# Kernel optimization log

Measured on AMD Instinct MI355X. Metric: run time of the kernel, lower is better.

Reference implementation:

```python
import jax, jax.numpy as jnp
import numpy as np

DILATIONS = [1, 2, 4, 8, 16, 32, 64, 128]
HIDDEN = 128
BATCH = 256
N_STEPS = 784
N_CLASSES = 10


def _drnn_layer(x_tbd, W_ih, W_hh, b_ih, b_hh, rate):
    """Dilated RNN layer. x_tbd: (T, B, D). Returns (T, B, H).

    Faithful to the repo's dRNN: pad T to a multiple of rate with zeros,
    fold each group of `rate` consecutive timesteps into the batch dim,
    step a tanh RNNCell over T/rate dilated steps (zero init state),
    then un-interleave back to (T, B, H).
    """
    T, B, D = x_tbd.shape
    n_dil = -(-T // rate)  # ceil division
    pad = n_dil * rate - T
    xp = jnp.pad(x_tbd, ((0, pad), (0, 0), (0, 0)))
    # (n_dil, rate*B, D): torch.cat of rate consecutive steps along batch
    xd = xp.reshape(n_dil, rate * B, D)

    def step(h, xt):
        h_new = jnp.tanh(xt @ W_ih.T + b_ih + h @ W_hh.T + b_hh)
        return h_new, h_new

    h0 = jnp.zeros((rate * B, W_ih.shape[0]), dtype=x_tbd.dtype)
    _, outs = jax.lax.scan(step, h0, xd)  # (n_dil, rate*B, H)
    outs = outs.reshape(n_dil * rate, B, -1)[:T]  # un-interleave, drop pad
    return outs


def _forward(x, Wih0, Whh0, bih0, bhh0, Wih, Whh, bih, bhh, W, b):
    # x: (B, T, D) -> time-major (T, B, D), matching _rnn_reformat
    h = jnp.transpose(x, (1, 0, 2))
    h = _drnn_layer(h, Wih0, Whh0, bih0, bhh0, DILATIONS[0])
    for i, rate in enumerate(DILATIONS[1:]):
        h = _drnn_layer(h, Wih[i], Whh[i], bih[i], bhh[i], rate)
    # dilations[0] == 1 branch: logits from last timestep of last layer
    return h[-1] @ W + b  # (B, n_classes)


def setup_inputs() -> dict:
    key = jax.random.key(0)
    ks = jax.random.split(key, 12)
    s = 0.05  # keep tanh in its linear-ish range
    return {
        "x": jax.random.normal(ks[0], (BATCH, N_STEPS, 1), jnp.float32),
        "Wih0": jax.random.normal(ks[1], (HIDDEN, 1), jnp.float32) * s,
        "Whh0": jax.random.normal(ks[2], (HIDDEN, HIDDEN), jnp.float32) * s,
        "bih0": jax.random.normal(ks[3], (HIDDEN,), jnp.float32) * s,
        "bhh0": jax.random.normal(ks[4], (HIDDEN,), jnp.float32) * s,
        "Wih": jax.random.normal(ks[5], (7, HIDDEN, HIDDEN), jnp.float32) * s,
        "Whh": jax.random.normal(ks[6], (7, HIDDEN, HIDDEN), jnp.float32) * s,
        "bih": jax.random.normal(ks[7], (7, HIDDEN), jnp.float32) * s,
        "bhh": jax.random.normal(ks[8], (7, HIDDEN), jnp.float32) * s,
        "W": jax.random.normal(ks[9], (HIDDEN, N_CLASSES), jnp.float32),
        "b": jax.random.normal(ks[10], (N_CLASSES,), jnp.float32),
    }


def reference(x, Wih0, Whh0, bih0, bhh0, Wih, Whh, bih, bhh, W, b):
    return _forward(x, Wih0, Whh0, bih0, bhh0, Wih, Whh, bih, bhh, W, b)
```

## Files before the change

kernel.cpp:

```cpp
#include <hip/hip_runtime.h>


typedef __attribute__((ext_vector_type(8))) short bf16x8;
typedef __attribute__((ext_vector_type(4))) float f32x4;
typedef __attribute__((ext_vector_type(2))) unsigned int u32x2;
typedef __attribute__((ext_vector_type(2))) unsigned long long u64x2;

#define TSTEPS 784
#define NBATCH 256
#define HID 128
#define SLOT_ELEMS (NBATCH * HID)
#define XPITCH 788
#define DYN_LDS 86016

struct Params {
  const float* x0;
  const float* Wih[8];
  const float* Whh[8];
  const float* bih[8];
  const float* bhh[8];
  unsigned short* phi[8];
  unsigned short* plo[8];
  float* hlast;
  int* flags;
  int jmax[8];
  int wpar[8];
  int sigb[8];
};

__device__ __forceinline__ unsigned short f32_to_bf16(float f) {
  unsigned int u = __builtin_bit_cast(unsigned int, f);
  u = (u + 0x7FFFu + ((u >> 16) & 1u)) >> 16;
  return (unsigned short)u;
}
__device__ __forceinline__ float bf16_to_f32(unsigned short s) {
  unsigned int u = ((unsigned int)s) << 16;
  return __builtin_bit_cast(float, u);
}
__device__ __forceinline__ void lds_barrier() {
  asm volatile("s_waitcnt lgkmcnt(0)" ::: "memory");
  __builtin_amdgcn_s_barrier();
  asm volatile("" ::: "memory");
}
__device__ __forceinline__ void load_wfrag(const float* __restrict__ p, bf16x8& hi, bf16x8& lo) {
#pragma unroll
  for (int i = 0; i < 8; ++i) {
    float v = p[i];
    unsigned short h = f32_to_bf16(v);
    float rem = v - bf16_to_f32(h);
    hi[i] = (short)h;
    lo[i] = (short)f32_to_bf16(rem);
  }
}

__global__ __launch_bounds__(256, 1) void drnn_fused(Params P) {
  extern __shared__ __align__(16) char smem[];
  unsigned short (*Hhi)[16][136] = (unsigned short(*)[16][136])smem;
  unsigned short (*Hlo)[16][136] = (unsigned short(*)[16][136])(smem + 8704);
  float* xlds = (float*)(smem + 17408);

  const int layer  = blockIdx.x >> 4;
  const int bg     = blockIdx.x & 15;
  const bool isL0   = (layer == 0);
  const bool isLast = (layer == 7);
  const int jmax = P.jmax[layer];
  const int wpar = P.wpar[layer];
  const int SIGB = P.sigb[layer];
  const float* __restrict__ Wih = P.Wih[layer];
  const float* __restrict__ Whh = P.Whh[layer];
  const float* __restrict__ bih = P.bih[layer];
  const float* __restrict__ bhh = P.bhh[layer];
  const unsigned short* __restrict__ Yin_hi = isL0 ? nullptr : P.phi[layer - 1];
  const unsigned short* __restrict__ Yin_lo = isL0 ? nullptr : P.plo[layer - 1];
  unsigned short* __restrict__ Yout_hi = isLast ? nullptr : P.phi[layer];
  unsigned short* __restrict__ Yout_lo = isLast ? nullptr : P.plo[layer];
  int* fin  = isL0 ? nullptr : P.flags + 64 * ((layer - 1) * 16 + bg);
  int* fout = isLast ? nullptr : P.flags + 64 * (layer * 16 + bg);

  const int tid  = threadIdx.x;
  const int wave = tid >> 6;
  const int lane = tid & 63;
  const int lrow = lane & 15;
  const int lgrp = lane >> 4;
  const int b0   = bg << 4;

  int seen = 0;
  auto wait_in = [&](int need) {
    if (seen >= need) return;
    while ((seen = __hip_atomic_load(fin, __ATOMIC_RELAXED,
                                     __HIP_MEMORY_SCOPE_SYSTEM)) < need)
      __builtin_amdgcn_s_sleep(2);
  };

  bf16x8 whhh[2][4], whhl[2][4], wihh[2][4], wihl[2][4];
#pragma unroll
  for (int tl = 0; tl < 2; ++tl) {
    const float* wp = Whh + (size_t)(wave * 32 + tl * 16 + lrow) * HID + lgrp * 8;
#pragma unroll
    for (int kb = 0; kb < 4; ++kb)
      load_wfrag(wp + kb * 32, whhh[tl][kb], whhl[tl][kb]);
  }
  if (!isL0) {
#pragma unroll
    for (int tl = 0; tl < 2; ++tl) {
      const float* wp = Wih + (size_t)(wave * 32 + tl * 16 + lrow) * HID + lgrp * 8;
#pragma unroll
      for (int kb = 0; kb < 4; ++kb)
        load_wfrag(wp + kb * 32, wihh[tl][kb], wihl[tl][kb]);
    }
  }
  f32x4 bias_[2], w0_[2];
#pragma unroll
  for (int tl = 0; tl < 2; ++tl)
#pragma unroll
    for (int r = 0; r < 4; ++r) {
      const int n = wave * 32 + tl * 16 + lgrp * 4 + r;
      bias_[tl][r] = bih[n] + bhh[n];
      w0_[tl][r]   = isL0 ? Wih[n] : 0.0f;
    }

  if (isL0) {
    for (int r = 0; r < 16; ++r)
      for (int i = tid; i < TSTEPS / 4; i += 256)
        *(f32x4*)&xlds[r * XPITCH + i * 4] =
            *(const f32x4*)&P.x0[(size_t)(b0 + r) * TSTEPS + i * 4];
    __syncthreads();
  }

  bf16x8 xhA[4], xlA[4], xhB[4], xlB[4];
  float xvA = 0.f, xvB = 0.f;
  const unsigned short* pin_h = nullptr;
  const unsigned short* pin_l = nullptr;
  if (isL0) {
    xvA = xlds[lrow * XPITCH + 0];
  } else {
    wait_in(1);
    const size_t lofs = ((size_t)b0 + lrow) * HID + lgrp * 8;
    pin_h = Yin_hi + lofs;
    pin_l = Yin_lo + lofs;
#pragma unroll
    for (int kb = 0; kb < 4; ++kb) {
      xhA[kb] = *(const bf16x8*)(pin_h + kb * 32);
      xlA[kb] = *(const bf16x8*)(pin_l + kb * 32);
    }
    pin_h += SLOT_ELEMS;
    pin_l += SLOT_ELEMS;
  }

  unsigned long long* wb_h = nullptr;
  unsigned long long* wb_l = nullptr;
  if (!isLast) {
    const int row = tid >> 4, cb = tid & 15;
    const size_t wofs = ((size_t)b0 + row) * HID + cb * 8;
    wb_h = (unsigned long long*)(Yout_hi + wofs);
    wb_l = (unsigned long long*)(Yout_lo + wofs);
  }
  const int wsrc = (tid >> 4) * 136 + (tid & 15) * 8;
  auto writeback = [&](int rp) {
    u64x2 vh = *(const u64x2*)((const unsigned short*)&Hhi[rp][0][0] + wsrc);
    u64x2 vl = *(const u64x2*)((const unsigned short*)&Hlo[rp][0][0] + wsrc);
    __hip_atomic_store(wb_h,     vh[0], __ATOMIC_RELAXED, __HIP_MEMORY_SCOPE_SYSTEM);
    __hip_atomic_store(wb_h + 1, vh[1], __ATOMIC_RELAXED, __HIP_MEMORY_SCOPE_SYSTEM);
    __hip_atomic_store(wb_l,     vl[0], __ATOMIC_RELAXED, __HIP_MEMORY_SCOPE_SYSTEM);
    __hip_atomic_store(wb_l + 1, vl[1], __ATOMIC_RELAXED, __HIP_MEMORY_SCOPE_SYSTEM);
    wb_h += SLOT_ELEMS / 4;
    wb_l += SLOT_ELEMS / 4;
  };
  auto signal = [&](int val) {
    asm volatile("s_waitcnt vmcnt(0)" ::: "memory");
    __builtin_amdgcn_s_barrier();
    if (tid == 0)
      __hip_atomic_store(fout, val, __ATOMIC_RELAXED, __HIP_MEMORY_SCOPE_SYSTEM);
  };

  int next_sig = SIGB;

  auto step = [&](int j, bf16x8 (&xh_c)[4], bf16x8 (&xl_c)[4],
                  bf16x8 (&xh_n)[4], bf16x8 (&xl_n)[4],
                  float& xv_c, float& xv_n) {
    if (j + 1 < jmax) {
      if (isL0) {
        xv_n = xlds[lrow * XPITCH + (j + 1)];
      } else {
        wait_in(j + 2);
#pragma unroll
        for (int kb = 0; kb < 4; ++kb) {
          xh_n[kb] = *(const bf16x8*)(pin_h + kb * 32);
          xl_n[kb] = *(const bf16x8*)(pin_l + kb * 32);
        }
        pin_h += SLOT_ELEMS;
        pin_l += SLOT_ELEMS;
      }
    }
    f32x4 c0[2], c1[2], c2[2];
#pragma unroll
    for (int tl = 0; tl < 2; ++tl) {
      c0[tl] = bias_[tl];
      c1[tl] = f32x4{0.f, 0.f, 0.f, 0.f};
      c2[tl] = f32x4{0.f, 0.f, 0.f, 0.f};
    }
    if (!isL0) {
#pragma unroll
      for (int kb = 0; kb < 4; ++kb)
#pragma unroll
        for (int tl = 0; tl < 2; ++tl) {
          c0[tl] = __builtin_amdgcn_mfma_f32_16x16x32_bf16(wihh[tl][kb], xh_c[kb], c0[tl], 0, 0, 0);
          c1[tl] = __builtin_amdgcn_mfma_f32_16x16x32_bf16(wihl[tl][kb], xh_c[kb], c1[tl], 0, 0, 0);
          c2[tl] = __builtin_amdgcn_mfma_f32_16x16x32_bf16(wihh[tl][kb], xl_c[kb], c2[tl], 0, 0, 0);
        }
    }
    if (j > 0) {
      lds_barrier();
      const int rp = (j - 1) & 1;
      bf16x8 bh[4], bl[4];
#pragma unroll
      for (int kb = 0; kb < 4; ++kb) {
        bh[kb] = *(const bf16x8*)&Hhi[rp][lrow][kb * 32 + lgrp * 8];
        bl[kb] = *(const bf16x8*)&Hlo[rp][lrow][kb * 32 + lgrp * 8];
      }
      if (!isLast && ((j - 1) & 1) == wpar) {
        const int wbslot = (j - 1 - wpar) >> 1;
        if (wbslot == next_sig) {
          signal(wbslot);
          next_sig += SIGB;
        }
        writeback(rp);
      }
#pragma unroll
      for (int kb = 0; kb < 4; ++kb)
#pragma unroll
        for (int tl = 0; tl < 2; ++tl) {
          c0[tl] = __builtin_amdgcn_mfma_f32_16x16x32_bf16(whhh[tl][kb], bh[kb], c0[tl], 0, 0, 0);
          c1[tl] = __builtin_amdgcn_mfma_f32_16x16x32_bf16(whhl[tl][kb], bh[kb], c1[tl], 0, 0, 0);
          c2[tl] = __builtin_amdgcn_mfma_f32_16x16x32_bf16(whhh[tl][kb], bl[kb], c2[tl], 0, 0, 0);
        }
    }
    const int pp = j & 1;
#pragma unroll
    for (int tl = 0; tl < 2; ++tl) {
      float y[4];
      f32x4 yv;
#pragma unroll
      for (int r = 0; r < 4; ++r) {
        float v = c0[tl][r] + c1[tl][r] + c2[tl][r];
        if (isL0) v = __builtin_fmaf(xv_c, w0_[tl][r], v);
        float t  = __builtin_amdgcn_exp2f(v * 2.885390081777927f);
        float rc = __builtin_amdgcn_rcpf(t + 1.0f);
        y[r] = __builtin_fmaf(-2.0f, rc, 1.0f);
        yv[r] = y[r];
      }
      float rem[4];
#pragma unroll
      for (int r = 0; r < 4; ++r) {
        float hf = __builtin_bit_cast(float,
            __builtin_bit_cast(unsigned int, y[r]) & 0xffff0000u);
        rem[r] = y[r] - hf;
      }
      u32x2 ph, pl;
      ph[0] = __builtin_amdgcn_perm(__builtin_bit_cast(unsigned int, y[1]),
                                    __builtin_bit_cast(unsigned int, y[0]), 0x07060302u);
      ph[1] = __builtin_amdgcn_perm(__builtin_bit_cast(unsigned int, y[3]),
                                    __builtin_bit_cast(unsigned int, y[2]), 0x07060302u);
      pl[0] = __builtin_amdgcn_perm(__builtin_bit_cast(unsigned int, rem[1]),
                                    __builtin_bit_cast(unsigned int, rem[0]), 0x07060302u);
      pl[1] = __builtin_amdgcn_perm(__builtin_bit_cast(unsigned int, rem[3]),
                                    __builtin_bit_cast(unsigned int, rem[2]), 0x07060302u);
      const int nb = wave * 32 + tl * 16 + lgrp * 4;
      *(u32x2*)&Hhi[pp][lrow][nb] = ph;
      *(u32x2*)&Hlo[pp][lrow][nb] = pl;
      if (isLast && j == jmax - 1)
        *(f32x4*)&P.hlast[(size_t)(b0 + lrow) * HID + nb] = yv;
    }
  };

  int j = 0;
  for (;;) {
    step(j, xhA, xlA, xhB, xlB, xvA, xvB);
    if (++j >= jmax) break;
    step(j, xhB, xlB, xhA, xlA, xvB, xvA);
    if (++j >= jmax) break;
  }

  if (!isLast) {
    if (((jmax - 1) & 1) == wpar) {
      lds_barrier();
      writeback((jmax - 1) & 1);
    }
    signal(((jmax - 1 - wpar) >> 1) + 1);
  }
}

__global__ __launch_bounds__(256) void logits_kernel(
    const float* __restrict__ hlast, const float* __restrict__ W,
    const float* __restrict__ bvec, float* __restrict__ out)
{
  __shared__ float Ws[HID * 10];
  const int tid = threadIdx.x;
  for (int i = tid; i < HID * 10; i += 256) Ws[i] = W[i];
  __syncthreads();
  float acc[10];
#pragma unroll
  for (int n = 0; n < 10; ++n) acc[n] = bvec[n];
  const float* h = hlast + (size_t)tid * HID;
#pragma unroll 4
  for (int k = 0; k < HID; ++k) {
    const float hv = h[k];
#pragma unroll
    for (int n = 0; n < 10; ++n) acc[n] += hv * Ws[k * 10 + n];
  }
#pragma unroll
  for (int n = 0; n < 10; ++n) out[(size_t)tid * 10 + n] = acc[n];
}

extern "C" void kernel_launch(void* const* d_in, const int* in_sizes, int n_in,
                              void* d_out, int out_size, void* d_ws, size_t ws_size,
                              hipStream_t stream) {
  (void)in_sizes; (void)n_in; (void)out_size; (void)ws_size;
  const float* x    = (const float*)d_in[0];
  const float* Wih0 = (const float*)d_in[1];
  const float* Whh0 = (const float*)d_in[2];
  const float* bih0 = (const float*)d_in[3];
  const float* bhh0 = (const float*)d_in[4];
  const float* WihA = (const float*)d_in[5];
  const float* WhhA = (const float*)d_in[6];
  const float* bihA = (const float*)d_in[7];
  const float* bhhA = (const float*)d_in[8];
  const float* Wout = (const float*)d_in[9];
  const float* bout = (const float*)d_in[10];
  float* out = (float*)d_out;

  static const int jmaxs[8] = {784, 392, 196, 98, 49, 25, 13, 7};
  static const int wpars[8] = {1, 1, 1, 1, 0, 0, 0, 0};
  static const int sigbs[8] = {8, 8, 8, 8, 4, 2, 2, 0};

  Params P;
  P.x0 = x;
  P.Wih[0] = Wih0; P.Whh[0] = Whh0; P.bih[0] = bih0; P.bhh[0] = bhh0;
  for (int i = 0; i < 7; ++i) {
    P.Wih[i + 1] = WihA + (size_t)i * HID * HID;
    P.Whh[i + 1] = WhhA + (size_t)i * HID * HID;
    P.bih[i + 1] = bihA + (size_t)i * HID;
    P.bhh[i + 1] = bhhA + (size_t)i * HID;
  }
  for (int i = 0; i < 8; ++i) {
    P.jmax[i] = jmaxs[i]; P.wpar[i] = wpars[i]; P.sigb[i] = sigbs[i];
  }

  unsigned short* wsp = (unsigned short*)d_ws;
  size_t off = 0;
  for (int i = 0; i < 7; ++i) {
    const size_t slots = (size_t)jmaxs[i + 1] * NBATCH * HID;
    P.phi[i] = wsp + off; off += slots;
    P.plo[i] = wsp + off; off += slots;
  }
  P.phi[7] = nullptr; P.plo[7] = nullptr;
  P.hlast = (float*)(wsp + off); off += (size_t)NBATCH * HID * 2;
  int* flags = (int*)(wsp + off);
  P.flags = flags;

  hipFuncSetAttribute((const void*)drnn_fused,
                      hipFuncAttributeMaxDynamicSharedMemorySize, DYN_LDS);

  hipMemsetAsync(flags, 0, 7 * 16 * 64 * sizeof(int), stream);
  drnn_fused<<<dim3(128), dim3(256), DYN_LDS, stream>>>(P);
  logits_kernel<<<dim3(1), dim3(256), 0, stream>>>(P.hlast, Wout, bout, out);
}
```

Baseline: 961.5 us.

## Switch recurrent MFMAs from split-bf16 3-pass to fp16 2-pass

Replaces the bf16 hi/lo split scheme (three MFMAs per tile: Whi*xhi, Wlo*xhi, Whi*xlo) with fp16 weights and an fp16 hi/lo split of activations only (two MFMAs per tile). Activations are split into fp16 hi plus fp16 residual, which works because tanh outputs and small weights fit fp16 range. The accumulators are regrouped per k-block into four independent chains to shorten MFMA dependency chains, and the hidden-state MFMAs are moved ahead of the writeback. This cuts MFMA count on the serial recurrence critical path and drops the low-part weight registers, at the cost of fp16 weight rounding precision.

```diff
diff --git a/kernel.cpp b/kernel.cpp
--- a/kernel.cpp
+++ b/kernel.cpp
@@ -1,9 +1,9 @@
 #include <hip/hip_runtime.h>
 
 
-typedef __attribute__((ext_vector_type(8))) short bf16x8;
+typedef __attribute__((ext_vector_type(8))) _Float16 f16x8;
+typedef __attribute__((ext_vector_type(4))) _Float16 f16x4;
 typedef __attribute__((ext_vector_type(4))) float f32x4;
-typedef __attribute__((ext_vector_type(2))) unsigned int u32x2;
 typedef __attribute__((ext_vector_type(2))) unsigned long long u64x2;
 
 #define TSTEPS 784
@@ -28,29 +28,21 @@
   int sigb[8];
 };
 
-__device__ __forceinline__ unsigned short f32_to_bf16(float f) {
-  unsigned int u = __builtin_bit_cast(unsigned int, f);
-  u = (u + 0x7FFFu + ((u >> 16) & 1u)) >> 16;
-  return (unsigned short)u;
-}
-__device__ __forceinline__ float bf16_to_f32(unsigned short s) {
-  unsigned int u = ((unsigned int)s) << 16;
-  return __builtin_bit_cast(float, u);
-}
 __device__ __forceinline__ void lds_barrier() {
   asm volatile("s_waitcnt lgkmcnt(0)" ::: "memory");
   __builtin_amdgcn_s_barrier();
   asm volatile("" ::: "memory");
 }
-__device__ __forceinline__ void load_wfrag(const float* __restrict__ p, bf16x8& hi, bf16x8& lo) {
-#pragma unroll
-  for (int i = 0; i < 8; ++i) {
-    float v = p[i];
-    unsigned short h = f32_to_bf16(v);
-    float rem = v - bf16_to_f32(h);
-    hi[i] = (short)h;
-    lo[i] = (short)f32_to_bf16(rem);
-  }
+__device__ __forceinline__ float tanh_fast(float v) {
+  float t  = __builtin_amdgcn_exp2f(v * 2.885390081777927f);
+  float rc = __builtin_amdgcn_rcpf(t + 1.0f);
+  return __builtin_fmaf(-2.0f, rc, 1.0f);
+}
+__device__ __forceinline__ f16x8 load_wf16(const float* __restrict__ p) {
+  f16x8 w;
+#pragma unroll
+  for (int i = 0; i < 8; ++i) w[i] = (_Float16)p[i];
+  return w;
 }
 
 __global__ __launch_bounds__(256, 1) void drnn_fused(Params P) {
@@ -92,13 +84,13 @@
       __builtin_amdgcn_s_sleep(2);
   };
 
-  bf16x8 whhh[2][4], whhl[2][4], wihh[2][4], wihl[2][4];
+  f16x8 whh[2][4], wih[2][4];
 #pragma unroll
   for (int tl = 0; tl < 2; ++tl) {
     const float* wp = Whh + (size_t)(wave * 32 + tl * 16 + lrow) * HID + lgrp * 8;
 #pragma unroll
     for (int kb = 0; kb < 4; ++kb)
-      load_wfrag(wp + kb * 32, whhh[tl][kb], whhl[tl][kb]);
+      whh[tl][kb] = load_wf16(wp + kb * 32);
   }
   if (!isL0) {
 #pragma unroll
@@ -106,7 +98,7 @@
       const float* wp = Wih + (size_t)(wave * 32 + tl * 16 + lrow) * HID + lgrp * 8;
 #pragma unroll
       for (int kb = 0; kb < 4; ++kb)
-        load_wfrag(wp + kb * 32, wihh[tl][kb], wihl[tl][kb]);
+        wih[tl][kb] = load_wf16(wp + kb * 32);
     }
   }
   f32x4 bias_[2], w0_[2];
@@ -127,7 +119,7 @@
     __syncthreads();
   }
 
-  bf16x8 xhA[4], xlA[4], xhB[4], xlB[4];
+  f16x8 xhA[4], xlA[4], xhB[4], xlB[4];
   float xvA = 0.f, xvB = 0.f;
   const unsigned short* pin_h = nullptr;
   const unsigned short* pin_l = nullptr;
@@ -140,8 +132,8 @@
     pin_l = Yin_lo + lofs;
 #pragma unroll
     for (int kb = 0; kb < 4; ++kb) {
-      xhA[kb] = *(const bf16x8*)(pin_h + kb * 32);
-      xlA[kb] = *(const bf16x8*)(pin_l + kb * 32);
+      xhA[kb] = *(const f16x8*)(pin_h + kb * 32);
+      xlA[kb] = *(const f16x8*)(pin_l + kb * 32);
     }
     pin_h += SLOT_ELEMS;
     pin_l += SLOT_ELEMS;
@@ -175,8 +167,8 @@
 
   int next_sig = SIGB;
 
-  auto step = [&](int j, bf16x8 (&xh_c)[4], bf16x8 (&xl_c)[4],
-                  bf16x8 (&xh_n)[4], bf16x8 (&xl_n)[4],
+  auto step = [&](int j, f16x8 (&xh_c)[4], f16x8 (&xl_c)[4],
+                  f16x8 (&xh_n)[4], f16x8 (&xl_n)[4],
                   float& xv_c, float& xv_n) {
     if (j + 1 < jmax) {
       if (isL0) {
@@ -185,39 +177,46 @@
         wait_in(j + 2);
 #pragma unroll
         for (int kb = 0; kb < 4; ++kb) {
-          xh_n[kb] = *(const bf16x8*)(pin_h + kb * 32);
-          xl_n[kb] = *(const bf16x8*)(pin_l + kb * 32);
+          xh_n[kb] = *(const f16x8*)(pin_h + kb * 32);
+          xl_n[kb] = *(const f16x8*)(pin_l + kb * 32);
         }
         pin_h += SLOT_ELEMS;
         pin_l += SLOT_ELEMS;
       }
     }
-    f32x4 c0[2], c1[2], c2[2];
+    f32x4 c[2][4];
 #pragma unroll
     for (int tl = 0; tl < 2; ++tl) {
-      c0[tl] = bias_[tl];
-      c1[tl] = f32x4{0.f, 0.f, 0.f, 0.f};
-      c2[tl] = f32x4{0.f, 0.f, 0.f, 0.f};
+      c[tl][0] = bias_[tl];
+#pragma unroll
+      for (int kb = 1; kb < 4; ++kb) c[tl][kb] = f32x4{0.f, 0.f, 0.f, 0.f};
     }
     if (!isL0) {
 #pragma unroll
       for (int kb = 0; kb < 4; ++kb)
 #pragma unroll
         for (int tl = 0; tl < 2; ++tl) {
-          c0[tl] = __builtin_amdgcn_mfma_f32_16x16x32_bf16(wihh[tl][kb], xh_c[kb], c0[tl], 0, 0, 0);
-          c1[tl] = __builtin_amdgcn_mfma_f32_16x16x32_bf16(wihl[tl][kb], xh_c[kb], c1[tl], 0, 0, 0);
-          c2[tl] = __builtin_amdgcn_mfma_f32_16x16x32_bf16(wihh[tl][kb], xl_c[kb], c2[tl], 0, 0, 0);
+          c[tl][kb] = __builtin_amdgcn_mfma_f32_16x16x32_f16(wih[tl][kb], xh_c[kb], c[tl][kb], 0, 0, 0);
+          c[tl][kb] = __builtin_amdgcn_mfma_f32_16x16x32_f16(wih[tl][kb], xl_c[kb], c[tl][kb], 0, 0, 0);
         }
     }
     if (j > 0) {
       lds_barrier();
       const int rp = (j - 1) & 1;
-      bf16x8 bh[4], bl[4];
-#pragma unroll
-      for (int kb = 0; kb < 4; ++kb) {
-        bh[kb] = *(const bf16x8*)&Hhi[rp][lrow][kb * 32 + lgrp * 8];
-        bl[kb] = *(const bf16x8*)&Hlo[rp][lrow][kb * 32 + lgrp * 8];
-      }
+      f16x8 bh[4], bl[4];
+#pragma unroll
+      for (int kb = 0; kb < 4; ++kb)
+        bh[kb] = *(const f16x8*)&Hhi[rp][lrow][kb * 32 + lgrp * 8];
+#pragma unroll
+      for (int kb = 0; kb < 4; ++kb)
+        bl[kb] = *(const f16x8*)&Hlo[rp][lrow][kb * 32 + lgrp * 8];
+#pragma unroll
+      for (int kb = 0; kb < 4; ++kb)
+#pragma unroll
+        for (int tl = 0; tl < 2; ++tl) {
+          c[tl][kb] = __builtin_amdgcn_mfma_f32_16x16x32_f16(whh[tl][kb], bh[kb], c[tl][kb], 0, 0, 0);
+          c[tl][kb] = __builtin_amdgcn_mfma_f32_16x16x32_f16(whh[tl][kb], bl[kb], c[tl][kb], 0, 0, 0);
+        }
       if (!isLast && ((j - 1) & 1) == wpar) {
         const int wbslot = (j - 1 - wpar) >> 1;
         if (wbslot == next_sig) {
@@ -226,48 +225,27 @@
         }
         writeback(rp);
       }
-#pragma unroll
-      for (int kb = 0; kb < 4; ++kb)
-#pragma unroll
-        for (int tl = 0; tl < 2; ++tl) {
-          c0[tl] = __builtin_amdgcn_mfma_f32_16x16x32_bf16(whhh[tl][kb], bh[kb], c0[tl], 0, 0, 0);
-          c1[tl] = __builtin_amdgcn_mfma_f32_16x16x32_bf16(whhl[tl][kb], bh[kb], c1[tl], 0, 0, 0);
-          c2[tl] = __builtin_amdgcn_mfma_f32_16x16x32_bf16(whhh[tl][kb], bl[kb], c2[tl], 0, 0, 0);
-        }
     }
     const int pp = j & 1;
 #pragma unroll
     for (int tl = 0; tl < 2; ++tl) {
-      float y[4];
+      f32x4 v = (c[tl][0] + c[tl][1]) + (c[tl][2] + c[tl][3]);
+      f16x4 h4, l4;
       f32x4 yv;
 #pragma unroll
       for (int r = 0; r < 4; ++r) {
-        float v = c0[tl][r] + c1[tl][r] + c2[tl][r];
-        if (isL0) v = __builtin_fmaf(xv_c, w0_[tl][r], v);
-        float t  = __builtin_amdgcn_exp2f(v * 2.885390081777927f);
-        float rc = __builtin_amdgcn_rcpf(t + 1.0f);
-        y[r] = __builtin_fmaf(-2.0f, rc, 1.0f);
-        yv[r] = y[r];
+        float vv = v[r];
+        if (isL0) vv = __builtin_fmaf(xv_c, w0_[tl][r], vv);
+        const float y = tanh_fast(vv);
+        yv[r] = y;
+        const _Float16 hh = (_Float16)y;
+        const float rem = y - (float)hh;
+        h4[r] = hh;
+        l4[r] = (_Float16)rem;
       }
-      float rem[4];
-#pragma unroll
-      for (int r = 0; r < 4; ++r) {
-        float hf = __builtin_bit_cast(float,
-            __builtin_bit_cast(unsigned int, y[r]) & 0xffff0000u);
-        rem[r] = y[r] - hf;
-      }
-      u32x2 ph, pl;
-      ph[0] = __builtin_amdgcn_perm(__builtin_bit_cast(unsigned int, y[1]),
-                                    __builtin_bit_cast(unsigned int, y[0]), 0x07060302u);
-      ph[1] = __builtin_amdgcn_perm(__builtin_bit_cast(unsigned int, y[3]),
-                                    __builtin_bit_cast(unsigned int, y[2]), 0x07060302u);
-      pl[0] = __builtin_amdgcn_perm(__builtin_bit_cast(unsigned int, rem[1]),
-                                    __builtin_bit_cast(unsigned int, rem[0]), 0x07060302u);
-      pl[1] = __builtin_amdgcn_perm(__builtin_bit_cast(unsigned int, rem[3]),
-                                    __builtin_bit_cast(unsigned int, rem[2]), 0x07060302u);
       const int nb = wave * 32 + tl * 16 + lgrp * 4;
-      *(u32x2*)&Hhi[pp][lrow][nb] = ph;
-      *(u32x2*)&Hlo[pp][lrow][nb] = pl;
+      *(f16x4*)&Hhi[pp][lrow][nb] = h4;
+      *(f16x4*)&Hlo[pp][lrow][nb] = l4;
       if (isLast && j == jmax - 1)
         *(f32x4*)&P.hlast[(size_t)(b0 + lrow) * HID + nb] = yv;
     }
```

Result: faster. 924.3 us (-3.9%).
